# Optimization experiments

Measured on AMD Instinct MI355X. Metric: run time of the kernel, lower is better.

Reference implementation:

```python
import jax, jax.numpy as jnp
import numpy as np

N = 1024      # layer_size (power of 2)
B = 16384     # batch
DEPTH = 2     # Butterfly depth (default)


def _abcd_offsets(n):
    """Factor sizes n, n/2, ..., 2 and their offsets into the packed ABCD buffer.
    A factor of size m has ABCD of shape (2, 2, m//2, 2) = 2m complex pairs."""
    offs = []
    off = 0
    m = n
    while m >= 2:
        offs.append((m, off))
        off += 2 * m
        m //= 2
    return offs, off  # off == 4n - 4


def setup_inputs() -> dict:
    key = jax.random.key(0)
    k1, k2, k3 = jax.random.split(key, 3)
    _, total = _abcd_offsets(N)
    x = jax.random.normal(k1, (B, N), jnp.float32)
    perm_logit = jax.random.normal(k2, (DEPTH, 3), jnp.float32)
    # scale ~1/sqrt(2) so the product of log2(n) random 2x2 blocks stays bounded
    abcd = jax.random.normal(k3, (DEPTH, total, 2), jnp.float32) * 0.7
    b = jnp.zeros((N,), jnp.float32)
    return {"x": x, "perm_logit": perm_logit, "abcd": abcd, "b": b}


def _perm_factor(h, p, m):
    """One BlockPerm factor (soft permutation) of size m applied blockwise.
    h: (B, n, 2) real/imag pairs. p: (3,) probabilities.
    p[0]: mix with even/odd separation; p[1], p[2]: mix each half with its reversal."""
    Bn, n, _ = h.shape
    h = h.reshape(Bn, n // m, m, 2)
    eo = jnp.concatenate([h[:, :, 0::2], h[:, :, 1::2]], axis=2)
    h = (1 - p[0]) * h + p[0] * eo
    h1, h2 = h[:, :, : m // 2], h[:, :, m // 2 :]
    h1 = (1 - p[1]) * h1 + p[1] * h1[:, :, ::-1]
    h2 = (1 - p[2]) * h2 + p[2] * h2[:, :, ::-1]
    return jnp.concatenate([h1, h2], axis=2).reshape(Bn, n, 2)


def _diag_factor(h, ABCD, m):
    """One Block2x2Diag factor of size m: out = [[A,B],[C,D]] x with diagonal A,B,C,D.
    h: (B, n, 2); ABCD: (2, 2, m//2, 2) complex pairs."""
    Bn, n, _ = h.shape
    hv = h.reshape(Bn, n // m, 2, m // 2, 2)  # (B, blocks, halves, m/2, cplx)
    xr, xi = hv[..., 0], hv[..., 1]
    Ar, Ai = ABCD[..., 0], ABCD[..., 1]
    yr = jnp.einsum('ijk,bnjk->bnik', Ar, xr) - jnp.einsum('ijk,bnjk->bnik', Ai, xi)
    yi = jnp.einsum('ijk,bnjk->bnik', Ar, xi) + jnp.einsum('ijk,bnjk->bnik', Ai, xr)
    return jnp.stack([yr, yi], axis=-1).reshape(Bn, n, 2)


def _forward(x, perm_logit, abcd, b):
    n = x.shape[-1]
    offs, _ = _abcd_offsets(n)
    # real_to_complex: (B, n) -> (B, n, 2)
    h = jnp.stack([x, jnp.zeros_like(x)], axis=-1)
    perm_sizes = [m for (m, _) in offs if m >= 4]
    depth = perm_logit.shape[0]
    for d in range(depth):
        # BlockPermProduct (share_logit=True): all factors share one (3,) logit
        p = jax.nn.sigmoid(perm_logit[d])
        for m in reversed(perm_sizes):      # smallest factor first
            h = _perm_factor(h, p, m)
        # Block2x2DiagProduct: factors applied smallest size first
        for (m, off) in reversed(offs):
            ABCD = abcd[d, off:off + 2 * m].reshape(2, 2, m // 2, 2)
            h = _diag_factor(h, ABCD, m)
    out = h[..., 0]  # take real part
    return b + out


def reference(x, perm_logit, abcd, b):
    return _forward(x, perm_logit, abcd, b)
```

## Files before the change

kernel.cpp:

```cpp
#include <hip/hip_runtime.h>
#include <hip/hip_bf16.h>
#include <stdint.h>

#define N_DIM 1024
#define DEPTH 2
#define ABCD_TOTAL 4092

typedef __attribute__((ext_vector_type(8))) short short8;
typedef __attribute__((ext_vector_type(4))) float floatx4;
typedef __attribute__((ext_vector_type(4))) float f4;

__device__ __forceinline__ f4 cmul(float cr, float ci, f4 v) {
    f4 r;
    r[0] = cr * v[0] - ci * v[1];
    r[1] = cr * v[1] + ci * v[0];
    r[2] = cr * v[2] - ci * v[3];
    r[3] = cr * v[3] + ci * v[2];
    return r;
}

__global__ __launch_bounds__(256) void build_and_cast(
    const float* __restrict__ perm_logit,
    const float* __restrict__ abcd,
    const float* __restrict__ x,
    __hip_bfloat16* __restrict__ S,
    __hip_bfloat16* __restrict__ xb)
{
    const int bx  = blockIdx.x;
    const int tid = threadIdx.x;
    __shared__ f4 h[2][N_DIM];

    if (bx >= 512) {
        const int cb = bx - 512;
        const size_t i = ((size_t)cb * 256 + tid) * 8;
        float4 v0 = *(const float4*)(x + i);
        float4 v1 = *(const float4*)(x + i + 4);
        union { __hip_bfloat16 e[8]; int4 v; } u;
        u.e[0] = __float2bfloat16(v0.x); u.e[1] = __float2bfloat16(v0.y);
        u.e[2] = __float2bfloat16(v0.z); u.e[3] = __float2bfloat16(v0.w);
        u.e[4] = __float2bfloat16(v1.x); u.e[5] = __float2bfloat16(v1.y);
        u.e[6] = __float2bfloat16(v1.z); u.e[7] = __float2bfloat16(v1.w);
        *(int4*)(xb + i) = u.v;
        return;
    }

    const int row0 = bx * 2;
    const f4 zz = {0.0f, 0.0f, 0.0f, 0.0f};
    for (int j = tid; j < N_DIM; j += 256) { h[0][j] = zz; h[1][j] = zz; }
    __syncthreads();
    if (tid == 0) {
        f4 e0 = {1.0f, 0.0f, 0.0f, 0.0f};
        f4 e1 = {0.0f, 0.0f, 1.0f, 0.0f};
        h[0][row0]     = e0;
        h[0][row0 + 1] = e1;
    }
    __syncthreads();

    int cur = 0;
    for (int d = 0; d < DEPTH; ++d) {
        const float p0 = 1.0f / (1.0f + expf(-perm_logit[d * 3 + 0]));
        const float p1 = 1.0f / (1.0f + expf(-perm_logit[d * 3 + 1]));
        const float p2 = 1.0f / (1.0f + expf(-perm_logit[d * 3 + 2]));

#pragma unroll
        for (int s = 2; s <= 10; ++s) {
            if (s >= 8) __syncthreads();
            else        __builtin_amdgcn_wave_barrier();
            const int half = 1 << (s - 1), hq = half >> 1;
            const int cnt   = (d == 0) ? half : 512;
            const int pbase = (d == 0) ? ((row0 >> s) << (s - 1)) : 0;
            const f4* __restrict__ in = h[cur];
            f4* __restrict__ out      = h[cur ^ 1];
            for (int tt = tid; tt < cnt; tt += 256) {
                const int t    = pbase + tt;
                const int blk  = t >> (s - 1);
                const int r    = t & (half - 1);
                const int base = blk << s;
                int q1, q2; float pc;
                if (r < hq) { q1 = r;           q2 = half - 1 - r;   pc = p1; }
                else        { int r2 = r - hq;  q1 = half + r2;
                              q2 = 2 * half - 1 - r2;                pc = p2; }
                const int src1 = (q1 < half) ? 2 * q1 : 2 * (q1 - half) + 1;
                const int src2 = (q2 < half) ? 2 * q2 : 2 * (q2 - half) + 1;
                f4 b1 = in[base + q1], a1 = in[base + src1];
                f4 b2 = in[base + q2], a2 = in[base + src2];
                f4 s1a = b1 + p0 * (a1 - b1);
                f4 s1b = b2 + p0 * (a2 - b2);
                out[base + q1] = s1a + pc * (s1b - s1a);
                out[base + q2] = s1b + pc * (s1a - s1b);
            }
            cur ^= 1;
        }
        __syncthreads();

        const float* __restrict__ abd = abcd + (size_t)d * (ABCD_TOTAL * 2);
#pragma unroll
        for (int s = 1; s <= 9; s += 2) {
            if (s == 9) __syncthreads();
            else        __builtin_amdgcn_wave_barrier();
            const int hh = 1 << (s - 1);
            const float* __restrict__ ab1 = abd + (size_t)(4096 - 8 * hh) * 2;
            const float* __restrict__ ab2 = abd + (size_t)(4096 - 16 * hh) * 2;
            const f4* __restrict__ in = h[cur];
            f4* __restrict__ out      = h[cur ^ 1];
            {
                const int g     = tid;
                const int k     = g & (hh - 1);
                const int base2 = (g >> (s - 1)) << (s + 1);
                f4 x0 = in[base2 + k];
                f4 x1 = in[base2 + k + hh];
                f4 x2 = in[base2 + k + 2 * hh];
                f4 x3 = in[base2 + k + 3 * hh];
                float2 A = *(const float2*)(ab1 + 2 * (size_t)k);
                float2 B = *(const float2*)(ab1 + 2 * (size_t)(hh + k));
                float2 C = *(const float2*)(ab1 + 2 * (size_t)(2 * hh + k));
                float2 D = *(const float2*)(ab1 + 2 * (size_t)(3 * hh + k));
                f4 y0 = cmul(A.x, A.y, x0) + cmul(B.x, B.y, x1);
                f4 y1 = cmul(C.x, C.y, x0) + cmul(D.x, D.y, x1);
                f4 y2 = cmul(A.x, A.y, x2) + cmul(B.x, B.y, x3);
                f4 y3 = cmul(C.x, C.y, x2) + cmul(D.x, D.y, x3);
                float2 A2 = *(const float2*)(ab2 + 2 * (size_t)k);
                float2 B2 = *(const float2*)(ab2 + 2 * (size_t)(2 * hh + k));
                float2 C2 = *(const float2*)(ab2 + 2 * (size_t)(4 * hh + k));
                float2 D2 = *(const float2*)(ab2 + 2 * (size_t)(6 * hh + k));
                float2 A3 = *(const float2*)(ab2 + 2 * (size_t)(hh + k));
                float2 B3 = *(const float2*)(ab2 + 2 * (size_t)(3 * hh + k));
                float2 C3 = *(const float2*)(ab2 + 2 * (size_t)(5 * hh + k));
                float2 D3 = *(const float2*)(ab2 + 2 * (size_t)(7 * hh + k));
                out[base2 + k]          = cmul(A2.x, A2.y, y0) + cmul(B2.x, B2.y, y2);
                out[base2 + k + 2 * hh] = cmul(C2.x, C2.y, y0) + cmul(D2.x, D2.y, y2);
                out[base2 + k + hh]     = cmul(A3.x, A3.y, y1) + cmul(B3.x, B3.y, y3);
                out[base2 + k + 3 * hh] = cmul(C3.x, C3.y, y1) + cmul(D3.x, D3.y, y3);
            }
            cur ^= 1;
        }
        __syncthreads();
    }

    for (int j = tid; j < N_DIM; j += 256) {
        f4 v = h[cur][j];
        S[(size_t)row0 * N_DIM + j]       = __float2bfloat16(v[0]);
        S[(size_t)(row0 + 1) * N_DIM + j] = __float2bfloat16(v[2]);
    }
}

__global__ __launch_bounds__(256) void transpose_w(
    const __hip_bfloat16* __restrict__ S, __hip_bfloat16* __restrict__ Wt)
{
    const int i0 = (blockIdx.x & 15) * 64;
    const int j0 = (blockIdx.x >> 4) * 64;
    __shared__ __hip_bfloat16 tile[64][72];
    const int r  = threadIdx.x >> 2;
    const int c0 = (threadIdx.x & 3) * 16;
    *(short8*)&tile[r][c0]     = *(const short8*)(S + (size_t)(i0 + r) * N_DIM + j0 + c0);
    *(short8*)&tile[r][c0 + 8] = *(const short8*)(S + (size_t)(i0 + r) * N_DIM + j0 + c0 + 8);
    __syncthreads();
    union { __hip_bfloat16 e[8]; short8 v; } o1, o2;
#pragma unroll
    for (int k = 0; k < 8; ++k) { o1.e[k] = tile[c0 + k][r]; o2.e[k] = tile[c0 + 8 + k][r]; }
    *(short8*)(Wt + (size_t)(j0 + r) * N_DIM + i0 + c0)     = o1.v;
    *(short8*)(Wt + (size_t)(j0 + r) * N_DIM + i0 + c0 + 8) = o2.v;
}

#define BM 128
#define BN 128
#define BK 64

__device__ __forceinline__ void gl_lds16(const void* g, void* l) {
    __builtin_amdgcn_global_load_lds(
        (const __attribute__((address_space(1))) uint32_t*)g,
        (__attribute__((address_space(3))) uint32_t*)l, 16, 0, 0);
}

__global__ __launch_bounds__(256, 4) void gemm_bt(
    const __hip_bfloat16* __restrict__ A,
    const __hip_bfloat16* __restrict__ Bt,
    const float* __restrict__ bias,
    float* __restrict__ C)
{
    const int tid = threadIdx.x;
    const int bx  = blockIdx.x;
    const int xcd = bx & 7;
    const int loc = bx >> 3;
    const int m0  = (xcd * 16 + (loc >> 3)) * BM;
    const int n0  = (loc & 7) * BN;

    __shared__ __hip_bfloat16 sA[BM * BK];
    __shared__ __hip_bfloat16 sB[BN * BK];

    const int lane = tid & 63;
    const int wm   = ((tid >> 6) & 1) * 64;
    const int wn   = ((tid >> 6) >> 1) * 64;
    const int lrow = lane & 15;
    const int lq   = lane >> 4;

    const int r1 = tid >> 3;
    const int cs = (tid & 7) ^ (r1 & 7);
    const int swz = lrow & 7;

    floatx4 acc[4][4] = {};

    for (int kt = 0; kt < 16; ++kt) {
        const int k0 = kt * BK;
#pragma unroll
        for (int i = 0; i < 4; ++i)
            gl_lds16(A + (size_t)(m0 + r1 + i * 32) * N_DIM + k0 + cs * 8,
                     (char*)sA + (tid + i * 256) * 16);
#pragma unroll
        for (int i = 0; i < 4; ++i)
            gl_lds16(Bt + (size_t)(n0 + r1 + i * 32) * N_DIM + k0 + cs * 8,
                     (char*)sB + (tid + i * 256) * 16);
        __syncthreads();

#pragma unroll
        for (int ks = 0; ks < 2; ++ks) {
            short8 af[4], bf[4];
            const int cc = (lq + 4 * ks) ^ swz;
#pragma unroll
            for (int i = 0; i < 4; ++i) {
                af[i] = *(const short8*)((const char*)sA + (((wm + i * 16 + lrow) * 8 + cc) * 16));
                bf[i] = *(const short8*)((const char*)sB + (((wn + i * 16 + lrow) * 8 + cc) * 16));
            }
#pragma unroll
            for (int i = 0; i < 4; ++i)
#pragma unroll
                for (int j = 0; j < 4; ++j)
                    acc[i][j] = __builtin_amdgcn_mfma_f32_16x16x32_bf16(
                        af[i], bf[j], acc[i][j], 0, 0, 0);
        }
        __syncthreads();
    }

#pragma unroll
    for (int j = 0; j < 4; ++j) {
        const int gn = n0 + wn + j * 16 + lrow;
        const float bv = bias[gn];
#pragma unroll
        for (int i = 0; i < 4; ++i) {
            const int gm = m0 + wm + i * 16 + lq * 4;
#pragma unroll
            for (int r = 0; r < 4; ++r)
                C[(size_t)(gm + r) * N_DIM + gn] = acc[i][j][r] + bv;
        }
    }
}

extern "C" void kernel_launch(void* const* d_in, const int* in_sizes, int n_in,
                              void* d_out, int out_size, void* d_ws, size_t ws_size,
                              hipStream_t stream) {
    const float* x          = (const float*)d_in[0];
    const float* perm_logit = (const float*)d_in[1];
    const float* abcd       = (const float*)d_in[2];
    const float* bias       = (const float*)d_in[3];
    float* out              = (float*)d_out;

    __hip_bfloat16* S  = (__hip_bfloat16*)d_out;
    __hip_bfloat16* Wt = (__hip_bfloat16*)d_ws;
    __hip_bfloat16* xb = (__hip_bfloat16*)((char*)d_ws + (1 << 21));

    build_and_cast<<<dim3(512 + 8192), dim3(256), 0, stream>>>(perm_logit, abcd, x, S, xb);
    transpose_w<<<dim3(256), dim3(256), 0, stream>>>(S, Wt);
    gemm_bt<<<dim3(1024), dim3(256), 0, stream>>>(xb, Wt, bias, out);
}
```

Measured before the change: 157.4 us.

## Replace GEMM with 256x256 tile, 8-wave, double-buffered pipelined MFMA kernel

Swaps the 128x128 single-buffered GEMM for a 256x256 tile kernel with 512 threads and double-buffered 128KB LDS. Global-to-LDS loads for the next K slices are interleaved with MFMA quadrants, using explicit vmcnt/lgkmcnt waits, barriers and setprio. The goal is to hide load latency and raise data reuse per tile. In exchange it launches only 256 blocks at low occupancy and depends on hand-tuned wait counts being correct.

```diff
diff --git a/kernel.cpp b/kernel.cpp
--- a/kernel.cpp
+++ b/kernel.cpp
@@ -162,85 +162,154 @@
     *(short8*)(Wt + (size_t)(j0 + r) * N_DIM + i0 + c0 + 8) = o2.v;
 }
 
-#define BM 128
-#define BN 128
-#define BK 64
-
 __device__ __forceinline__ void gl_lds16(const void* g, void* l) {
     __builtin_amdgcn_global_load_lds(
         (const __attribute__((address_space(1))) uint32_t*)g,
         (__attribute__((address_space(3))) uint32_t*)l, 16, 0, 0);
 }
 
-__global__ __launch_bounds__(256, 4) void gemm_bt(
+#define GBAR  __builtin_amdgcn_s_barrier()
+#define LGKM0 do { asm volatile("s_waitcnt lgkmcnt(0)" ::: "memory"); \
+                   __builtin_amdgcn_sched_barrier(0); } while (0)
+#define VM4   asm volatile("s_waitcnt vmcnt(4)" ::: "memory")
+#define VM0   asm volatile("s_waitcnt vmcnt(0)" ::: "memory")
+#define PRIO1 __builtin_amdgcn_s_setprio(1)
+#define PRIO0 __builtin_amdgcn_s_setprio(0)
+
+#define STG_A(kelem, h, buf) do { \
+    gl_lds16(gA + (kelem) + (size_t)((h) * 128)      * N_DIM, sA + (buf) * 32768 + (h) * 16384 + tb); \
+    gl_lds16(gA + (kelem) + (size_t)((h) * 128 + 64) * N_DIM, sA + (buf) * 32768 + (h) * 16384 + 8192 + tb); \
+  } while (0)
+#define STG_B(kelem, h, buf) do { \
+    gl_lds16(gB + (kelem) + (size_t)((h) * 128)      * N_DIM, sB + (buf) * 32768 + (h) * 16384 + tb); \
+    gl_lds16(gB + (kelem) + (size_t)((h) * 128 + 64) * N_DIM, sB + (buf) * 32768 + (h) * 16384 + 8192 + tb); \
+  } while (0)
+
+#define RD_A(buf, mq) do { \
+    _Pragma("unroll") \
+    for (int fi = 0; fi < 4; ++fi) { \
+      af[fi][0] = *(const short8*)(aRd + (buf) * 32768 + (mq) * 8192 + fi * 2048 + cp0); \
+      af[fi][1] = *(const short8*)(aRd + (buf) * 32768 + (mq) * 8192 + fi * 2048 + cp1); \
+    } } while (0)
+
+#define RD_B(buf, nq) do { \
+    _Pragma("unroll") \
+    for (int n = 0; n < 2; ++n) { \
+      bf[nq][n][0] = *(const short8*)(bRd + (buf) * 32768 + ((nq) * 2 + n) * 2048 + cp0); \
+      bf[nq][n][1] = *(const short8*)(bRd + (buf) * 32768 + ((nq) * 2 + n) * 2048 + cp1); \
+    } } while (0)
+
+#define MM16(mq, nq) do { \
+    _Pragma("unroll") \
+    for (int fi = 0; fi < 4; ++fi) { \
+      _Pragma("unroll") \
+      for (int n = 0; n < 2; ++n) { \
+        acc[(mq) * 4 + fi][(nq) * 2 + n] = __builtin_amdgcn_mfma_f32_16x16x32_bf16( \
+            af[fi][0], bf[nq][n][0], acc[(mq) * 4 + fi][(nq) * 2 + n], 0, 0, 0); \
+        acc[(mq) * 4 + fi][(nq) * 2 + n] = __builtin_amdgcn_mfma_f32_16x16x32_bf16( \
+            af[fi][1], bf[nq][n][1], acc[(mq) * 4 + fi][(nq) * 2 + n], 0, 0, 0); \
+      } } } while (0)
+
+__global__ __launch_bounds__(512, 2) void gemm_256(
     const __hip_bfloat16* __restrict__ A,
     const __hip_bfloat16* __restrict__ Bt,
     const float* __restrict__ bias,
     float* __restrict__ C)
 {
-    const int tid = threadIdx.x;
-    const int bx  = blockIdx.x;
-    const int xcd = bx & 7;
-    const int loc = bx >> 3;
-    const int m0  = (xcd * 16 + (loc >> 3)) * BM;
-    const int n0  = (loc & 7) * BN;
-
-    __shared__ __hip_bfloat16 sA[BM * BK];
-    __shared__ __hip_bfloat16 sB[BN * BK];
-
-    const int lane = tid & 63;
-    const int wm   = ((tid >> 6) & 1) * 64;
-    const int wn   = ((tid >> 6) >> 1) * 64;
-    const int lrow = lane & 15;
+    __shared__ __attribute__((aligned(128))) char smem[131072];
+
+    const int t    = threadIdx.x;
+    const int bid  = blockIdx.x;
+    const int xcd  = bid & 7;
+    const int loc  = bid >> 3;
+    const int m0   = (xcd * 8 + (loc >> 2)) * 256;
+    const int n0   = (loc & 3) * 256;
+
+    const int lane = t & 63;
+    const int wave = t >> 6;
+    const int wm   = wave >> 2;
+    const int wn   = wave & 3;
     const int lq   = lane >> 4;
-
-    const int r1 = tid >> 3;
-    const int cs = (tid & 7) ^ (r1 & 7);
-    const int swz = lrow & 7;
-
-    floatx4 acc[4][4] = {};
-
-    for (int kt = 0; kt < 16; ++kt) {
-        const int k0 = kt * BK;
-#pragma unroll
-        for (int i = 0; i < 4; ++i)
-            gl_lds16(A + (size_t)(m0 + r1 + i * 32) * N_DIM + k0 + cs * 8,
-                     (char*)sA + (tid + i * 256) * 16);
-#pragma unroll
-        for (int i = 0; i < 4; ++i)
-            gl_lds16(Bt + (size_t)(n0 + r1 + i * 32) * N_DIM + k0 + cs * 8,
-                     (char*)sB + (tid + i * 256) * 16);
-        __syncthreads();
-
-#pragma unroll
-        for (int ks = 0; ks < 2; ++ks) {
-            short8 af[4], bf[4];
-            const int cc = (lq + 4 * ks) ^ swz;
-#pragma unroll
-            for (int i = 0; i < 4; ++i) {
-                af[i] = *(const short8*)((const char*)sA + (((wm + i * 16 + lrow) * 8 + cc) * 16));
-                bf[i] = *(const short8*)((const char*)sB + (((wn + i * 16 + lrow) * 8 + cc) * 16));
-            }
-#pragma unroll
-            for (int i = 0; i < 4; ++i)
-#pragma unroll
-                for (int j = 0; j < 4; ++j)
-                    acc[i][j] = __builtin_amdgcn_mfma_f32_16x16x32_bf16(
-                        af[i], bf[j], acc[i][j], 0, 0, 0);
-        }
-        __syncthreads();
-    }
-
-#pragma unroll
-    for (int j = 0; j < 4; ++j) {
-        const int gn = n0 + wn + j * 16 + lrow;
-        const float bv = bias[gn];
-#pragma unroll
-        for (int i = 0; i < 4; ++i) {
-            const int gm = m0 + wm + i * 16 + lq * 4;
+    const int l15  = lane & 15;
+
+    const int r8 = t >> 3;
+    const int cl = (t & 7) ^ (r8 & 7);
+    const __hip_bfloat16* gA = A  + (size_t)(m0 + r8) * N_DIM + cl * 8;
+    const __hip_bfloat16* gB = Bt + (size_t)(n0 + r8) * N_DIM + cl * 8;
+
+    char* const sA = smem;
+    char* const sB = smem + 65536;
+    const int tb = t * 16;
+
+    const char* aRd = smem + wm * 16384 + l15 * 128;
+    const char* bRd = smem + 65536 + (wn >> 1) * 16384 + ((wn & 1) * 64 + l15) * 128;
+    const int cp0 = ((lq)     ^ (lane & 7)) * 16;
+    const int cp1 = ((4 + lq) ^ (lane & 7)) * 16;
+
+    short8  af[4][2];
+    short8  bf[2][2][2];
+    floatx4 acc[8][4] = {};
+
+    STG_A(0, 0, 0); STG_A(0, 1, 0); STG_B(0, 0, 0); STG_B(0, 1, 0);
+    STG_B(64, 0, 1); STG_A(64, 0, 1);
+    VM4;
+    GBAR;
+
+    for (int it = 0; it < 7; ++it) {
+        const int k0 = it * 128;
+        RD_A(0, 0); RD_B(0, 0);
+        STG_A(k0 + 64, 1, 1);
+        GBAR; LGKM0; PRIO1; MM16(0, 0); PRIO0; GBAR;
+        RD_B(0, 1);
+        STG_B(k0 + 64, 1, 1);
+        GBAR; LGKM0; PRIO1; MM16(0, 1); PRIO0; GBAR;
+        RD_A(0, 1);
+        STG_B(k0 + 128, 0, 0);
+        GBAR; LGKM0; PRIO1; MM16(1, 0); PRIO0; GBAR;
+        STG_A(k0 + 128, 0, 0);
+        GBAR; LGKM0; PRIO1; MM16(1, 1); PRIO0; VM4; GBAR;
+        RD_A(1, 0); RD_B(1, 0);
+        STG_A(k0 + 128, 1, 0);
+        GBAR; LGKM0; PRIO1; MM16(0, 0); PRIO0; GBAR;
+        RD_B(1, 1);
+        STG_B(k0 + 128, 1, 0);
+        GBAR; LGKM0; PRIO1; MM16(0, 1); PRIO0; GBAR;
+        RD_A(1, 1);
+        STG_B(k0 + 192, 0, 1);
+        GBAR; LGKM0; PRIO1; MM16(1, 0); PRIO0; GBAR;
+        STG_A(k0 + 192, 0, 1);
+        GBAR; LGKM0; PRIO1; MM16(1, 1); PRIO0; VM4; GBAR;
+    }
+
+    {
+        RD_A(0, 0); RD_B(0, 0);
+        STG_A(896 + 64, 1, 1);
+        GBAR; LGKM0; PRIO1; MM16(0, 0); PRIO0; GBAR;
+        RD_B(0, 1);
+        STG_B(896 + 64, 1, 1);
+        GBAR; LGKM0; PRIO1; MM16(0, 1); PRIO0; GBAR;
+        RD_A(0, 1);
+        GBAR; LGKM0; PRIO1; MM16(1, 0); PRIO0; GBAR;
+        GBAR; LGKM0; PRIO1; MM16(1, 1); PRIO0; VM0; GBAR;
+        RD_A(1, 0); RD_B(1, 0);
+        GBAR; LGKM0; PRIO1; MM16(0, 0); PRIO0; GBAR;
+        RD_B(1, 1);
+        GBAR; LGKM0; PRIO1; MM16(0, 1); PRIO0; GBAR;
+        RD_A(1, 1);
+        GBAR; LGKM0; PRIO1; MM16(1, 0); PRIO0; GBAR;
+        PRIO1; MM16(1, 1); PRIO0;
+    }
+
+#pragma unroll
+    for (int f = 0; f < 8; ++f) {
+        const int gm = m0 + wm * 128 + f * 16 + lq * 4;
+#pragma unroll
+        for (int nf = 0; nf < 4; ++nf) {
+            const int gn = n0 + wn * 64 + nf * 16 + l15;
+            const float bv = bias[gn];
 #pragma unroll
             for (int r = 0; r < 4; ++r)
-                C[(size_t)(gm + r) * N_DIM + gn] = acc[i][j][r] + bv;
+                C[(size_t)(gm + r) * N_DIM + gn] = acc[f][nf][r] + bv;
         }
     }
 }
@@ -260,5 +329,5 @@
 
     build_and_cast<<<dim3(512 + 8192), dim3(256), 0, stream>>>(perm_logit, abcd, x, S, xb);
     transpose_w<<<dim3(256), dim3(256), 0, stream>>>(S, Wt);
-    gemm_bt<<<dim3(1024), dim3(256), 0, stream>>>(xb, Wt, bias, out);
-}
+    gemm_256<<<dim3(256), dim3(512), 0, stream>>>(xb, Wt, bias, out);
+}
```

After: 153.4 us, median of 2. -2.5%, faster.
